# Performance work log

Measured on AMD Instinct MI355X. Metric: run time of the kernel, lower is better.

The kernel has to match this reference:

```python
import jax, jax.numpy as jnp
import numpy as np

B, T, A, FA = 4, 1024, 8, 16   # batch, frames, animals, per-animal feat
C, H, L = 1024, 16, 8          # n_embd, n_head, n_layer
D_IN, D_OUT = A * FA, 256


def _ln(x, g, b, eps=1e-5):
    mu = x.mean(-1, keepdims=True)
    var = ((x - mu) ** 2).mean(-1, keepdims=True)
    return (x - mu) * jax.lax.rsqrt(var + eps) * g + b


def setup_inputs() -> dict:
    key = jax.random.key(0)
    ks = iter(jax.random.split(key, 32))
    w = lambda shape: jax.random.normal(next(ks), shape, jnp.float32) * 0.02
    inp = {
        'tokens': jax.random.normal(next(ks), (B, T, A, FA), jnp.float32),
        'tok_emb_w': w((D_IN, C)), 'tok_emb_b': jnp.zeros((C,), jnp.float32),
        # per-layer params stacked along leading n_layer axis
        'ln1_g': jnp.ones((L, C), jnp.float32), 'ln1_b': jnp.zeros((L, C), jnp.float32),
        'Wq': w((L, C, C)), 'bq': jnp.zeros((L, C), jnp.float32),
        'Wk': w((L, C, C)), 'bk': jnp.zeros((L, C), jnp.float32),
        'Wv': w((L, C, C)), 'bv': jnp.zeros((L, C), jnp.float32),
        'Wo': w((L, C, C)), 'bo': jnp.zeros((L, C), jnp.float32),
        'ln2_g': jnp.ones((L, C), jnp.float32), 'ln2_b': jnp.zeros((L, C), jnp.float32),
        'W1': w((L, C, 4 * C)), 'b1': jnp.zeros((L, 4 * C), jnp.float32),
        'W2': w((L, 4 * C, C)), 'b2': jnp.zeros((L, C), jnp.float32),
        'lnf_g': jnp.ones((C,), jnp.float32), 'lnf_b': jnp.zeros((C,), jnp.float32),
        'proj_w': w((C, D_OUT)), 'proj_b': jnp.zeros((D_OUT,), jnp.float32),
        'dec_w1': w((D_OUT, D_OUT)), 'dec_b1': jnp.zeros((D_OUT,), jnp.float32),
        'dec_ln_g': jnp.ones((D_OUT,), jnp.float32), 'dec_ln_b': jnp.zeros((D_OUT,), jnp.float32),
        'dec_w2': w((D_OUT, D_IN)), 'dec_b2': jnp.zeros((D_IN,), jnp.float32),
    }
    return inp


def reference(tokens, tok_emb_w, tok_emb_b, ln1_g, ln1_b, Wq, bq, Wk, bk, Wv, bv,
              Wo, bo, ln2_g, ln2_b, W1, b1, W2, b2, lnf_g, lnf_b, proj_w, proj_b,
              dec_w1, dec_b1, dec_ln_g, dec_ln_b, dec_w2, dec_b2):
    b, t = tokens.shape[0], tokens.shape[1]
    x = tokens.reshape(b, t, -1)                      # (B,T,D_IN) flatten(2)
    h = x @ tok_emb_w + tok_emb_b                     # (B,T,C)
    mask = jnp.tril(jnp.ones((t, t), bool))           # causal mask
    dh = C // H
    scale = 1.0 / np.sqrt(dh)

    def layer(h, p):
        g1, bb1, wq, bq_, wk, bk_, wv, bv_, wo, bo_, g2, bb2, w1, b1_, w2, b2_ = p
        a = _ln(h, g1, bb1)
        q = (a @ wq + bq_).reshape(b, t, H, dh).transpose(0, 2, 1, 3)
        k = (a @ wk + bk_).reshape(b, t, H, dh).transpose(0, 2, 1, 3)
        v = (a @ wv + bv_).reshape(b, t, H, dh).transpose(0, 2, 1, 3)
        att = jnp.einsum('bhqd,bhkd->bhqk', q, k) * scale
        att = jnp.where(mask, att, -jnp.inf)
        att = jax.nn.softmax(att, axis=-1)
        y = jnp.einsum('bhqk,bhkd->bhqd', att, v)
        y = y.transpose(0, 2, 1, 3).reshape(b, t, C)
        h = h + (y @ wo + bo_)
        m = _ln(h, g2, bb2)
        h = h + jax.nn.gelu(m @ w1 + b1_, approximate=False) @ w2 + b2_
        return h, None

    h, _ = jax.lax.scan(layer, h, (ln1_g, ln1_b, Wq, bq, Wk, bk, Wv, bv, Wo, bo,
                                   ln2_g, ln2_b, W1, b1, W2, b2))
    feats = _ln(h, lnf_g, lnf_b) @ proj_w + proj_b    # (B,T,D_OUT)
    # decode=True path: decoder_frame then frame-delta prediction
    pred = _ln(jnp.tanh(feats @ dec_w1 + dec_b1), dec_ln_g, dec_ln_b) @ dec_w2 + dec_b2
    return pred[:, :-1] - x[:, 1:]                    # (B,T-1,D_IN)
```

## Files before the change

### kernel.cpp

```cpp
#include <hip/hip_runtime.h>
#include <hip/hip_bf16.h>

typedef unsigned short u16;
typedef __attribute__((ext_vector_type(8))) short bf16x8;
typedef __attribute__((ext_vector_type(4))) float f32x4;

#define BT     4096
#define CDIM   1024
#define NH     16
#define FF     4096
#define DIN    128
#define DOUT   256
#define NLAYER 8
#define TSEQ   1024
#define NBATCH 4

__device__ inline u16 f2bfu(float v) {
    __hip_bfloat16 h = __float2bfloat16(v);
    return __builtin_bit_cast(unsigned short, h);
}

__device__ inline void async_copy16(const u16* g, u16* l) {
    __builtin_amdgcn_global_load_lds((const __attribute__((address_space(1))) void*)g,
                                     (__attribute__((address_space(3))) void*)l,
                                     16, 0, 0);
}

template<int ACT, int RES, int OBF>
__global__ __launch_bounds__(256) void gemm_bt(
    const u16* __restrict__ A, const u16* __restrict__ Bt,
    const float* __restrict__ bias, const float* res,
    void* outp, int M, int N, int K)
{
    __shared__ __align__(16) u16 As[128 * 32];
    __shared__ __align__(16) u16 Bs[128 * 32];
    int tid  = threadIdx.x;
    int wave = tid >> 6, lane = tid & 63;
    int ln = lane & 15, quad = lane >> 4;
    int wm = (wave >> 1) * 64, wn = (wave & 1) * 64;
    const u16* Ab = A  + (size_t)blockIdx.y * 128 * K;
    const u16* Bb = Bt + (size_t)blockIdx.x * 128 * K;
    f32x4 acc[4][4] = {};
    for (int kt = 0; kt < K; kt += 32) {
#pragma unroll
        for (int it = 0; it < 2; ++it) {
            int e = it * 256 + tid;
            int row = e >> 2, col = (e & 3) * 8;
            int lbase = (it * 256 + wave * 64) * 8;
            async_copy16(Ab + (size_t)row * K + kt + col, As + lbase);
            async_copy16(Bb + (size_t)row * K + kt + col, Bs + lbase);
        }
        __syncthreads();
        bf16x8 af[4], bfr[4];
#pragma unroll
        for (int i = 0; i < 4; ++i)
            af[i] = *(const bf16x8*)&As[(wm + i * 16 + ln) * 32 + quad * 8];
#pragma unroll
        for (int j = 0; j < 4; ++j)
            bfr[j] = *(const bf16x8*)&Bs[(wn + j * 16 + ln) * 32 + quad * 8];
#pragma unroll
        for (int i = 0; i < 4; ++i)
#pragma unroll
            for (int j = 0; j < 4; ++j)
                acc[i][j] = __builtin_amdgcn_mfma_f32_16x16x32_bf16(af[i], bfr[j], acc[i][j], 0, 0, 0);
        __syncthreads();
    }
    int gr0 = blockIdx.y * 128 + wm + quad * 4;
    int gc0 = blockIdx.x * 128 + wn + ln;
#pragma unroll
    for (int i = 0; i < 4; ++i) {
#pragma unroll
        for (int j = 0; j < 4; ++j) {
            int gc = gc0 + j * 16;
            float bv = bias[gc];
#pragma unroll
            for (int r = 0; r < 4; ++r) {
                int gr = gr0 + i * 16 + r;
                float v = acc[i][j][r] + bv;
                if (ACT == 1) v = 0.5f * v * (1.0f + erff(v * 0.70710678118654752f));
                if (ACT == 2) v = tanhf(v);
                size_t idx = (size_t)gr * N + gc;
                if (RES) v += res[idx];
                if (OBF) ((u16*)outp)[idx] = f2bfu(v);
                else     ((float*)outp)[idx] = v;
            }
        }
    }
}

__global__ __launch_bounds__(64) void attn_kernel(const u16* __restrict__ qkv, u16* __restrict__ y)
{
    __shared__ __align__(16) u16 Plds[16 * 32];
    int qt = blockIdx.x, bh = blockIdx.y;
    int b = bh >> 4, h = bh & 15;
    int q0 = qt * 16;
    int lane = threadIdx.x;
    int ln = lane & 15, quad = lane >> 4;
    const int SC = 3 * CDIM;
    const u16* base = qkv + (size_t)b * TSEQ * SC;
    const u16* qrow = base + (size_t)(q0 + ln) * SC + h * 64 + quad * 8;
    bf16x8 qf0 = *(const bf16x8*)(qrow);
    bf16x8 qf1 = *(const bf16x8*)(qrow + 32);
    f32x4 O[4] = {};
    float m_i[4], l_i[4];
#pragma unroll
    for (int r = 0; r < 4; ++r) { m_i[r] = -1e30f; l_i[r] = 0.0f; }
    int nkt = qt / 2 + 1;
    for (int kt = 0; kt < nkt; ++kt) {
        int j0 = kt * 32;
        const u16* krow0 = base + (size_t)(j0 + ln) * SC + CDIM + h * 64;
        const u16* krow1 = base + (size_t)(j0 + 16 + ln) * SC + CDIM + h * 64;
        bf16x8 kf00 = *(const bf16x8*)(krow0 + quad * 8);
        bf16x8 kf01 = *(const bf16x8*)(krow0 + 32 + quad * 8);
        bf16x8 kf10 = *(const bf16x8*)(krow1 + quad * 8);
        bf16x8 kf11 = *(const bf16x8*)(krow1 + 32 + quad * 8);
        f32x4 S0 = {}, S1 = {};
        S0 = __builtin_amdgcn_mfma_f32_16x16x32_bf16(qf0, kf00, S0, 0, 0, 0);
        S0 = __builtin_amdgcn_mfma_f32_16x16x32_bf16(qf1, kf01, S0, 0, 0, 0);
        S1 = __builtin_amdgcn_mfma_f32_16x16x32_bf16(qf0, kf10, S1, 0, 0, 0);
        S1 = __builtin_amdgcn_mfma_f32_16x16x32_bf16(qf1, kf11, S1, 0, 0, 0);
        bool needmask = (j0 + 32 > q0);
        float alpha[4];
#pragma unroll
        for (int r = 0; r < 4; ++r) {
            float s0 = S0[r] * 0.125f, s1 = S1[r] * 0.125f;
            if (needmask) {
                int qr = q0 + quad * 4 + r;
                if (j0 + ln > qr)      s0 = -1e30f;
                if (j0 + 16 + ln > qr) s1 = -1e30f;
            }
            float mx = fmaxf(s0, s1);
            mx = fmaxf(mx, __shfl_xor(mx, 1));
            mx = fmaxf(mx, __shfl_xor(mx, 2));
            mx = fmaxf(mx, __shfl_xor(mx, 4));
            mx = fmaxf(mx, __shfl_xor(mx, 8));
            float mn = fmaxf(m_i[r], mx);
            float al = __expf(m_i[r] - mn);
            float p0 = __expf(s0 - mn);
            float p1 = __expf(s1 - mn);
            float rs = p0 + p1;
            rs += __shfl_xor(rs, 1);
            rs += __shfl_xor(rs, 2);
            rs += __shfl_xor(rs, 4);
            rs += __shfl_xor(rs, 8);
            l_i[r] = l_i[r] * al + rs;
            m_i[r] = mn;
            alpha[r] = al;
            Plds[(quad * 4 + r) * 32 + ln]      = f2bfu(p0);
            Plds[(quad * 4 + r) * 32 + 16 + ln] = f2bfu(p1);
        }
#pragma unroll
        for (int nt = 0; nt < 4; ++nt)
#pragma unroll
            for (int r = 0; r < 4; ++r)
                O[nt][r] *= alpha[r];
        __syncthreads();
        bf16x8 pa = *(const bf16x8*)&Plds[ln * 32 + quad * 8];
        const u16* vrow = base + (size_t)(j0 + quad * 8) * SC + 2 * CDIM + h * 64 + ln;
#pragma unroll
        for (int nt = 0; nt < 4; ++nt) {
            bf16x8 vf;
#pragma unroll
            for (int jj = 0; jj < 8; ++jj)
                vf[jj] = (short)vrow[(size_t)jj * SC + nt * 16];
            O[nt] = __builtin_amdgcn_mfma_f32_16x16x32_bf16(pa, vf, O[nt], 0, 0, 0);
        }
        __syncthreads();
    }
#pragma unroll
    for (int r = 0; r < 4; ++r) {
        float invl = 1.0f / l_i[r];
        int row = q0 + quad * 4 + r;
#pragma unroll
        for (int nt = 0; nt < 4; ++nt)
            y[(size_t)(b * TSEQ + row) * CDIM + h * 64 + nt * 16 + ln] = f2bfu(O[nt][r] * invl);
    }
}

template<int NPT>
__global__ __launch_bounds__(256) void ln_kernel(const float* __restrict__ x,
    const float* __restrict__ g, const float* __restrict__ bet, u16* __restrict__ out)
{
    const int n = NPT * 256;
    int row = blockIdx.x, tid = threadIdx.x;
    const float* xr = x + (size_t)row * n;
    float xv[NPT];
    float s1 = 0.f, s2 = 0.f;
#pragma unroll
    for (int k = 0; k < NPT; ++k) {
        float v = xr[k * 256 + tid];
        xv[k] = v; s1 += v; s2 += v * v;
    }
#pragma unroll
    for (int m = 1; m < 64; m <<= 1) { s1 += __shfl_xor(s1, m); s2 += __shfl_xor(s2, m); }
    __shared__ float red[8];
    int wv = tid >> 6;
    if ((tid & 63) == 0) { red[wv] = s1; red[4 + wv] = s2; }
    __syncthreads();
    s1 = red[0] + red[1] + red[2] + red[3];
    s2 = red[4] + red[5] + red[6] + red[7];
    float mu = s1 * (1.0f / n);
    float var = s2 * (1.0f / n) - mu * mu;
    float rs = rsqrtf(var + 1e-5f);
#pragma unroll
    for (int k = 0; k < NPT; ++k) {
        int c = k * 256 + tid;
        out[(size_t)row * n + c] = f2bfu((xv[k] - mu) * rs * g[c] + bet[c]);
    }
}

__device__ inline void tile_tc(const float* src, u16* dst, int K, int N, int kt, int nt,
                               int tid, float* sm)
{
    int c = tid & 31, r0 = tid >> 5;
#pragma unroll
    for (int rr = r0; rr < 32; rr += 8)
        sm[rr * 33 + c] = src[(size_t)(kt * 32 + rr) * N + nt * 32 + c];
    __syncthreads();
#pragma unroll
    for (int rr = r0; rr < 32; rr += 8)
        dst[(size_t)(nt * 32 + rr) * K + kt * 32 + c] = f2bfu(sm[c * 33 + rr]);
}

__global__ __launch_bounds__(256) void transpose_cvt(const float* __restrict__ src,
    u16* __restrict__ dst, int K, int N)
{
    __shared__ float sm[32 * 33];
    tile_tc(src, dst, K, N, blockIdx.y, blockIdx.x, threadIdx.x, sm);
}

__global__ __launch_bounds__(256) void prep_layer(
    const float* __restrict__ Wq, const float* __restrict__ Wk, const float* __restrict__ Wv,
    const float* __restrict__ Wo, const float* __restrict__ W1, const float* __restrict__ W2,
    const float* __restrict__ bq, const float* __restrict__ bk, const float* __restrict__ bv,
    u16* __restrict__ qkv_t, u16* __restrict__ wo_t, u16* __restrict__ w1_t,
    u16* __restrict__ w2_t, float* __restrict__ bias3)
{
    __shared__ float sm[32 * 33];
    int id = blockIdx.x, tid = threadIdx.x;
    const float* src; u16* dst; int K, N, kt, nt;
    if (id < 3072) {
        int w = id >> 10, t = id & 1023;
        src = (w == 0) ? Wq : ((w == 1) ? Wk : Wv);
        dst = qkv_t + (size_t)w * CDIM * CDIM;
        K = CDIM; N = CDIM; kt = t >> 5; nt = t & 31;
    } else if (id < 4096) {
        int t = id - 3072; src = Wo; dst = wo_t; K = CDIM; N = CDIM; kt = t >> 5; nt = t & 31;
    } else if (id < 8192) {
        int t = id - 4096; src = W1; dst = w1_t; K = CDIM; N = FF;   kt = t >> 7; nt = t & 127;
    } else {
        int t = id - 8192; src = W2; dst = w2_t; K = FF;   N = CDIM; kt = t >> 5; nt = t & 31;
    }
    tile_tc(src, dst, K, N, kt, nt, tid, sm);
    if (id < 3) {
        const float* bsrc = (id == 0) ? bq : ((id == 1) ? bk : bv);
        for (int k2 = tid; k2 < CDIM; k2 += 256) bias3[id * CDIM + k2] = bsrc[k2];
    }
}

__global__ __launch_bounds__(256) void cvt_bf16(const float* __restrict__ src,
    u16* __restrict__ dst, int n)
{
    int i = blockIdx.x * 256 + threadIdx.x;
    if (i < n) dst[i] = f2bfu(src[i]);
}

__global__ __launch_bounds__(256) void out_sub(const float* __restrict__ pred,
    const float* __restrict__ x, float* __restrict__ out, int total)
{
    int i = blockIdx.x * 256 + threadIdx.x;
    if (i >= total) return;
    int b = i / ((TSEQ - 1) * DIN);
    int rtmp = i - b * (TSEQ - 1) * DIN;
    int t = rtmp >> 7, f = rtmp & 127;
    out[i] = pred[(size_t)(b * TSEQ + t) * DIN + f] - x[(size_t)(b * TSEQ + t + 1) * DIN + f];
}

__global__ void fail_flag(float* out) { if (threadIdx.x == 0 && blockIdx.x == 0) out[0] = 1.0e6f; }

extern "C" void kernel_launch(void* const* d_in, const int* in_sizes, int n_in,
                              void* d_out, int out_size, void* d_ws, size_t ws_size,
                              hipStream_t stream)
{
    (void)in_sizes; (void)n_in; (void)out_size;
    const float* tokens    = (const float*)d_in[0];
    const float* tok_emb_w = (const float*)d_in[1];
    const float* tok_emb_b = (const float*)d_in[2];
    const float* ln1_g = (const float*)d_in[3];
    const float* ln1_b = (const float*)d_in[4];
    const float* Wq = (const float*)d_in[5];
    const float* bq = (const float*)d_in[6];
    const float* Wk = (const float*)d_in[7];
    const float* bk = (const float*)d_in[8];
    const float* Wv = (const float*)d_in[9];
    const float* bv = (const float*)d_in[10];
    const float* Wo = (const float*)d_in[11];
    const float* bo = (const float*)d_in[12];
    const float* ln2_g = (const float*)d_in[13];
    const float* ln2_b = (const float*)d_in[14];
    const float* W1 = (const float*)d_in[15];
    const float* b1 = (const float*)d_in[16];
    const float* W2 = (const float*)d_in[17];
    const float* b2 = (const float*)d_in[18];
    const float* lnf_g = (const float*)d_in[19];
    const float* lnf_b = (const float*)d_in[20];
    const float* proj_w = (const float*)d_in[21];
    const float* proj_b = (const float*)d_in[22];
    const float* dec_w1 = (const float*)d_in[23];
    const float* dec_b1 = (const float*)d_in[24];
    const float* dec_ln_g = (const float*)d_in[25];
    const float* dec_ln_b = (const float*)d_in[26];
    const float* dec_w2 = (const float*)d_in[27];
    const float* dec_b2 = (const float*)d_in[28];

    char* p = (char*)d_ws;
    auto alloc = [&](size_t bytes) -> char* {
        char* r = p; p += (bytes + 255) & ~(size_t)255; return r;
    };
    u16*   xb     = (u16*)  alloc((size_t)BT * DIN * 2);
    float* h      = (float*)alloc((size_t)BT * CDIM * 4);
    u16*   abuf   = (u16*)  alloc((size_t)BT * CDIM * 2);
    u16*   qkvb   = (u16*)  alloc((size_t)BT * 3 * CDIM * 2);
    u16*   yb     = (u16*)  alloc((size_t)BT * CDIM * 2);
    u16*   t1     = (u16*)  alloc((size_t)BT * FF * 2);
    u16*   feats  = (u16*)  alloc((size_t)BT * DOUT * 2);
    float* d1     = (float*)alloc((size_t)BT * DOUT * 4);
    u16*   d1n    = (u16*)  alloc((size_t)BT * DOUT * 2);
    float* pred   = (float*)alloc((size_t)BT * DIN * 4);
    u16*   emb_t  = (u16*)  alloc((size_t)CDIM * DIN * 2);
    u16*   proj_t = (u16*)  alloc((size_t)DOUT * CDIM * 2);
    u16*   dec1_t = (u16*)  alloc((size_t)DOUT * DOUT * 2);
    u16*   dec2_t = (u16*)  alloc((size_t)DIN * DOUT * 2);
    u16*   qkv_t  = (u16*)  alloc((size_t)3 * CDIM * CDIM * 2);
    u16*   wo_t   = (u16*)  alloc((size_t)CDIM * CDIM * 2);
    u16*   w1_t   = (u16*)  alloc((size_t)FF * CDIM * 2);
    u16*   w2_t   = (u16*)  alloc((size_t)CDIM * FF * 2);
    float* bias3  = (float*)alloc((size_t)3 * CDIM * 4);
    if ((size_t)(p - (char*)d_ws) > ws_size) {
        fail_flag<<<1, 64, 0, stream>>>((float*)d_out);
        return;
    }

    cvt_bf16<<<(BT * DIN) / 256, 256, 0, stream>>>(tokens, xb, BT * DIN);
    transpose_cvt<<<dim3(CDIM / 32, DIN / 32),  256, 0, stream>>>(tok_emb_w, emb_t,  DIN,  CDIM);
    transpose_cvt<<<dim3(DOUT / 32, CDIM / 32), 256, 0, stream>>>(proj_w,    proj_t, CDIM, DOUT);
    transpose_cvt<<<dim3(DOUT / 32, DOUT / 32), 256, 0, stream>>>(dec_w1,    dec1_t, DOUT, DOUT);
    transpose_cvt<<<dim3(DIN / 32,  DOUT / 32), 256, 0, stream>>>(dec_w2,    dec2_t, DOUT, DIN);
    gemm_bt<0, 0, 0><<<dim3(CDIM / 128, BT / 128), 256, 0, stream>>>(
        xb, emb_t, tok_emb_b, nullptr, h, BT, CDIM, DIN);

    for (int l = 0; l < NLAYER; ++l) {
        prep_layer<<<12288, 256, 0, stream>>>(
            Wq + (size_t)l * CDIM * CDIM, Wk + (size_t)l * CDIM * CDIM,
            Wv + (size_t)l * CDIM * CDIM, Wo + (size_t)l * CDIM * CDIM,
            W1 + (size_t)l * CDIM * FF,   W2 + (size_t)l * FF * CDIM,
            bq + l * CDIM, bk + l * CDIM, bv + l * CDIM,
            qkv_t, wo_t, w1_t, w2_t, bias3);
        ln_kernel<4><<<BT, 256, 0, stream>>>(h, ln1_g + l * CDIM, ln1_b + l * CDIM, abuf);
        gemm_bt<0, 0, 1><<<dim3(3 * CDIM / 128, BT / 128), 256, 0, stream>>>(
            abuf, qkv_t, bias3, nullptr, qkvb, BT, 3 * CDIM, CDIM);
        attn_kernel<<<dim3(TSEQ / 16, NBATCH * NH), 64, 0, stream>>>(qkvb, yb);
        gemm_bt<0, 1, 0><<<dim3(CDIM / 128, BT / 128), 256, 0, stream>>>(
            yb, wo_t, bo + l * CDIM, h, h, BT, CDIM, CDIM);
        ln_kernel<4><<<BT, 256, 0, stream>>>(h, ln2_g + l * CDIM, ln2_b + l * CDIM, abuf);
        gemm_bt<1, 0, 1><<<dim3(FF / 128, BT / 128), 256, 0, stream>>>(
            abuf, w1_t, b1 + l * FF, nullptr, t1, BT, FF, CDIM);
        gemm_bt<0, 1, 0><<<dim3(CDIM / 128, BT / 128), 256, 0, stream>>>(
            t1, w2_t, b2 + l * CDIM, h, h, BT, CDIM, FF);
    }

    ln_kernel<4><<<BT, 256, 0, stream>>>(h, lnf_g, lnf_b, abuf);
    gemm_bt<0, 0, 1><<<dim3(DOUT / 128, BT / 128), 256, 0, stream>>>(
        abuf, proj_t, proj_b, nullptr, feats, BT, DOUT, CDIM);
    gemm_bt<2, 0, 0><<<dim3(DOUT / 128, BT / 128), 256, 0, stream>>>(
        feats, dec1_t, dec_b1, nullptr, d1, BT, DOUT, DOUT);
    ln_kernel<1><<<BT, 256, 0, stream>>>(d1, dec_ln_g, dec_ln_b, d1n);
    gemm_bt<0, 0, 0><<<dim3(DIN / 128, BT / 128), 256, 0, stream>>>(
        d1n, dec2_t, dec_b2, nullptr, pred, BT, DIN, DOUT);
    int total = NBATCH * (TSEQ - 1) * DIN;
    out_sub<<<(total + 255) / 256, 256, 0, stream>>>(pred, tokens, (float*)d_out, total);
}
```

Baseline: 3.264 ms.

## Split-K atomics for residual GEMMs, transposed V layout, 32-row attention tiles

```diff
diff --git a/kernel.cpp b/kernel.cpp
--- a/kernel.cpp
+++ b/kernel.cpp
@@ -26,11 +26,11 @@
                                      16, 0, 0);
 }
 
-template<int ACT, int RES, int OBF>
+template<int ACT, int RES, int OBF, int EPI>
 __global__ __launch_bounds__(256) void gemm_bt(
     const u16* __restrict__ A, const u16* __restrict__ Bt,
     const float* __restrict__ bias, const float* res,
-    void* outp, int M, int N, int K)
+    void* outp, u16* __restrict__ vtp, int N, int K, int Kc)
 {
     __shared__ __align__(16) u16 As[128 * 32];
     __shared__ __align__(16) u16 Bs[128 * 32];
@@ -38,10 +38,11 @@
     int wave = tid >> 6, lane = tid & 63;
     int ln = lane & 15, quad = lane >> 4;
     int wm = (wave >> 1) * 64, wn = (wave & 1) * 64;
+    int k0 = blockIdx.z * Kc;
     const u16* Ab = A  + (size_t)blockIdx.y * 128 * K;
     const u16* Bb = Bt + (size_t)blockIdx.x * 128 * K;
     f32x4 acc[4][4] = {};
-    for (int kt = 0; kt < K; kt += 32) {
+    for (int kt = k0; kt < k0 + Kc; kt += 32) {
 #pragma unroll
         for (int it = 0; it < 2; ++it) {
             int e = it * 256 + tid;
@@ -72,109 +73,136 @@
 #pragma unroll
         for (int j = 0; j < 4; ++j) {
             int gc = gc0 + j * 16;
-            float bv = bias[gc];
+            float bv = (EPI == 1) ? ((blockIdx.z == 0) ? bias[gc] : 0.0f) : bias[gc];
 #pragma unroll
             for (int r = 0; r < 4; ++r) {
                 int gr = gr0 + i * 16 + r;
                 float v = acc[i][j][r] + bv;
                 if (ACT == 1) v = 0.5f * v * (1.0f + erff(v * 0.70710678118654752f));
                 if (ACT == 2) v = tanhf(v);
-                size_t idx = (size_t)gr * N + gc;
-                if (RES) v += res[idx];
-                if (OBF) ((u16*)outp)[idx] = f2bfu(v);
-                else     ((float*)outp)[idx] = v;
+                if (EPI == 1) {
+                    unsafeAtomicAdd(&((float*)outp)[(size_t)gr * N + gc], v);
+                } else if (EPI == 2) {
+                    if ((int)blockIdx.x < 16) {
+                        ((u16*)outp)[(size_t)gr * 2048 + gc] = f2bfu(v);
+                    } else {
+                        int c2 = gc - 2048;
+                        int hh = c2 >> 6, f = c2 & 63;
+                        int bb = gr >> 10, t = gr & 1023;
+                        vtp[((size_t)(bb * 16 + hh) * 64 + f) * TSEQ + t] = f2bfu(v);
+                    }
+                } else {
+                    size_t idx = (size_t)gr * N + gc;
+                    if (RES) v += res[idx];
+                    if (OBF) ((u16*)outp)[idx] = f2bfu(v);
+                    else     ((float*)outp)[idx] = v;
+                }
             }
         }
     }
 }
 
-__global__ __launch_bounds__(64) void attn_kernel(const u16* __restrict__ qkv, u16* __restrict__ y)
-{
-    __shared__ __align__(16) u16 Plds[16 * 32];
+__global__ __launch_bounds__(64) void attn_kernel(const u16* __restrict__ qk,
+    const u16* __restrict__ vT, u16* __restrict__ y)
+{
+    __shared__ __align__(16) u16 Plds[2][16 * 32];
     int qt = blockIdx.x, bh = blockIdx.y;
     int b = bh >> 4, h = bh & 15;
-    int q0 = qt * 16;
+    int q0 = qt * 32;
     int lane = threadIdx.x;
     int ln = lane & 15, quad = lane >> 4;
-    const int SC = 3 * CDIM;
-    const u16* base = qkv + (size_t)b * TSEQ * SC;
-    const u16* qrow = base + (size_t)(q0 + ln) * SC + h * 64 + quad * 8;
-    bf16x8 qf0 = *(const bf16x8*)(qrow);
-    bf16x8 qf1 = *(const bf16x8*)(qrow + 32);
-    f32x4 O[4] = {};
-    float m_i[4], l_i[4];
-#pragma unroll
-    for (int r = 0; r < 4; ++r) { m_i[r] = -1e30f; l_i[r] = 0.0f; }
-    int nkt = qt / 2 + 1;
+    const u16* qbase = qk + (size_t)b * TSEQ * 2048;
+    bf16x8 qf[2][2];
+#pragma unroll
+    for (int qi = 0; qi < 2; ++qi) {
+        const u16* qrow = qbase + (size_t)(q0 + qi * 16 + ln) * 2048 + h * 64 + quad * 8;
+        qf[qi][0] = *(const bf16x8*)qrow;
+        qf[qi][1] = *(const bf16x8*)(qrow + 32);
+    }
+    const u16* vbase = vT + (size_t)bh * 64 * TSEQ;
+    f32x4 O[2][4] = {};
+    float m_i[2][4], l_i[2][4];
+#pragma unroll
+    for (int qi = 0; qi < 2; ++qi)
+#pragma unroll
+        for (int r = 0; r < 4; ++r) { m_i[qi][r] = -1e30f; l_i[qi][r] = 0.0f; }
+    int nkt = qt + 1;
     for (int kt = 0; kt < nkt; ++kt) {
         int j0 = kt * 32;
-        const u16* krow0 = base + (size_t)(j0 + ln) * SC + CDIM + h * 64;
-        const u16* krow1 = base + (size_t)(j0 + 16 + ln) * SC + CDIM + h * 64;
-        bf16x8 kf00 = *(const bf16x8*)(krow0 + quad * 8);
-        bf16x8 kf01 = *(const bf16x8*)(krow0 + 32 + quad * 8);
-        bf16x8 kf10 = *(const bf16x8*)(krow1 + quad * 8);
-        bf16x8 kf11 = *(const bf16x8*)(krow1 + 32 + quad * 8);
-        f32x4 S0 = {}, S1 = {};
-        S0 = __builtin_amdgcn_mfma_f32_16x16x32_bf16(qf0, kf00, S0, 0, 0, 0);
-        S0 = __builtin_amdgcn_mfma_f32_16x16x32_bf16(qf1, kf01, S0, 0, 0, 0);
-        S1 = __builtin_amdgcn_mfma_f32_16x16x32_bf16(qf0, kf10, S1, 0, 0, 0);
-        S1 = __builtin_amdgcn_mfma_f32_16x16x32_bf16(qf1, kf11, S1, 0, 0, 0);
-        bool needmask = (j0 + 32 > q0);
-        float alpha[4];
+        bf16x8 kf[2][2];
+#pragma unroll
+        for (int kk = 0; kk < 2; ++kk) {
+            const u16* krow = qbase + (size_t)(j0 + kk * 16 + ln) * 2048 + 1024 + h * 64 + quad * 8;
+            kf[kk][0] = *(const bf16x8*)krow;
+            kf[kk][1] = *(const bf16x8*)(krow + 32);
+        }
+        f32x4 S[2][2] = {};
+#pragma unroll
+        for (int qi = 0; qi < 2; ++qi)
+#pragma unroll
+            for (int kk = 0; kk < 2; ++kk) {
+                S[qi][kk] = __builtin_amdgcn_mfma_f32_16x16x32_bf16(qf[qi][0], kf[kk][0], S[qi][kk], 0, 0, 0);
+                S[qi][kk] = __builtin_amdgcn_mfma_f32_16x16x32_bf16(qf[qi][1], kf[kk][1], S[qi][kk], 0, 0, 0);
+            }
+        bool lastt = (kt == qt);
+        float alpha[2][4];
+#pragma unroll
+        for (int qi = 0; qi < 2; ++qi) {
+#pragma unroll
+            for (int r = 0; r < 4; ++r) {
+                float s0 = S[qi][0][r] * 0.125f, s1 = S[qi][1][r] * 0.125f;
+                if (lastt) {
+                    int qr = q0 + qi * 16 + quad * 4 + r;
+                    if (j0 + ln > qr)      s0 = -1e30f;
+                    if (j0 + 16 + ln > qr) s1 = -1e30f;
+                }
+                float mx = fmaxf(s0, s1);
+                mx = fmaxf(mx, __shfl_xor(mx, 1));
+                mx = fmaxf(mx, __shfl_xor(mx, 2));
+                mx = fmaxf(mx, __shfl_xor(mx, 4));
+                mx = fmaxf(mx, __shfl_xor(mx, 8));
+                float mn = fmaxf(m_i[qi][r], mx);
+                float al = __expf(m_i[qi][r] - mn);
+                float p0 = __expf(s0 - mn);
+                float p1 = __expf(s1 - mn);
+                float rs = p0 + p1;
+                rs += __shfl_xor(rs, 1);
+                rs += __shfl_xor(rs, 2);
+                rs += __shfl_xor(rs, 4);
+                rs += __shfl_xor(rs, 8);
+                l_i[qi][r] = l_i[qi][r] * al + rs;
+                m_i[qi][r] = mn;
+                alpha[qi][r] = al;
+                Plds[qi][(quad * 4 + r) * 32 + ln]      = f2bfu(p0);
+                Plds[qi][(quad * 4 + r) * 32 + 16 + ln] = f2bfu(p1);
+            }
+#pragma unroll
+            for (int nt = 0; nt < 4; ++nt)
+#pragma unroll
+                for (int r = 0; r < 4; ++r)
+                    O[qi][nt][r] *= alpha[qi][r];
+        }
+        __syncthreads();
+        bf16x8 pa0 = *(const bf16x8*)&Plds[0][ln * 32 + quad * 8];
+        bf16x8 pa1 = *(const bf16x8*)&Plds[1][ln * 32 + quad * 8];
+#pragma unroll
+        for (int nt = 0; nt < 4; ++nt) {
+            bf16x8 vf = *(const bf16x8*)(vbase + (size_t)(nt * 16 + ln) * TSEQ + j0 + quad * 8);
+            O[0][nt] = __builtin_amdgcn_mfma_f32_16x16x32_bf16(pa0, vf, O[0][nt], 0, 0, 0);
+            O[1][nt] = __builtin_amdgcn_mfma_f32_16x16x32_bf16(pa1, vf, O[1][nt], 0, 0, 0);
+        }
+        __syncthreads();
+    }
+#pragma unroll
+    for (int qi = 0; qi < 2; ++qi)
 #pragma unroll
         for (int r = 0; r < 4; ++r) {
-            float s0 = S0[r] * 0.125f, s1 = S1[r] * 0.125f;
-            if (needmask) {
-                int qr = q0 + quad * 4 + r;
-                if (j0 + ln > qr)      s0 = -1e30f;
-                if (j0 + 16 + ln > qr) s1 = -1e30f;
-            }
-            float mx = fmaxf(s0, s1);
-            mx = fmaxf(mx, __shfl_xor(mx, 1));
-            mx = fmaxf(mx, __shfl_xor(mx, 2));
-            mx = fmaxf(mx, __shfl_xor(mx, 4));
-            mx = fmaxf(mx, __shfl_xor(mx, 8));
-            float mn = fmaxf(m_i[r], mx);
-            float al = __expf(m_i[r] - mn);
-            float p0 = __expf(s0 - mn);
-            float p1 = __expf(s1 - mn);
-            float rs = p0 + p1;
-            rs += __shfl_xor(rs, 1);
-            rs += __shfl_xor(rs, 2);
-            rs += __shfl_xor(rs, 4);
-            rs += __shfl_xor(rs, 8);
-            l_i[r] = l_i[r] * al + rs;
-            m_i[r] = mn;
-            alpha[r] = al;
-            Plds[(quad * 4 + r) * 32 + ln]      = f2bfu(p0);
-            Plds[(quad * 4 + r) * 32 + 16 + ln] = f2bfu(p1);
-        }
-#pragma unroll
-        for (int nt = 0; nt < 4; ++nt)
-#pragma unroll
-            for (int r = 0; r < 4; ++r)
-                O[nt][r] *= alpha[r];
-        __syncthreads();
-        bf16x8 pa = *(const bf16x8*)&Plds[ln * 32 + quad * 8];
-        const u16* vrow = base + (size_t)(j0 + quad * 8) * SC + 2 * CDIM + h * 64 + ln;
-#pragma unroll
-        for (int nt = 0; nt < 4; ++nt) {
-            bf16x8 vf;
-#pragma unroll
-            for (int jj = 0; jj < 8; ++jj)
-                vf[jj] = (short)vrow[(size_t)jj * SC + nt * 16];
-            O[nt] = __builtin_amdgcn_mfma_f32_16x16x32_bf16(pa, vf, O[nt], 0, 0, 0);
-        }
-        __syncthreads();
-    }
-#pragma unroll
-    for (int r = 0; r < 4; ++r) {
-        float invl = 1.0f / l_i[r];
-        int row = q0 + quad * 4 + r;
-#pragma unroll
-        for (int nt = 0; nt < 4; ++nt)
-            y[(size_t)(b * TSEQ + row) * CDIM + h * 64 + nt * 16 + ln] = f2bfu(O[nt][r] * invl);
-    }
+            float invl = 1.0f / l_i[qi][r];
+            int row = q0 + qi * 16 + quad * 4 + r;
+#pragma unroll
+            for (int nt = 0; nt < 4; ++nt)
+                y[(size_t)(b * TSEQ + row) * CDIM + h * 64 + nt * 16 + ln] = f2bfu(O[qi][nt][r] * invl);
+        }
 }
 
 template<int NPT>
@@ -263,6 +291,12 @@
 {
     int i = blockIdx.x * 256 + threadIdx.x;
     if (i < n) dst[i] = f2bfu(src[i]);
+}
+
+__global__ __launch_bounds__(256) void zero_f32(float* __restrict__ dst, int n)
+{
+    int i = blockIdx.x * 256 + threadIdx.x;
+    if (i < n) dst[i] = 0.0f;
 }
 
 __global__ __launch_bounds__(256) void out_sub(const float* __restrict__ pred,
@@ -317,25 +351,27 @@
     auto alloc = [&](size_t bytes) -> char* {
         char* r = p; p += (bytes + 255) & ~(size_t)255; return r;
     };
-    u16*   xb     = (u16*)  alloc((size_t)BT * DIN * 2);
-    float* h      = (float*)alloc((size_t)BT * CDIM * 4);
-    u16*   abuf   = (u16*)  alloc((size_t)BT * CDIM * 2);
-    u16*   qkvb   = (u16*)  alloc((size_t)BT * 3 * CDIM * 2);
-    u16*   yb     = (u16*)  alloc((size_t)BT * CDIM * 2);
-    u16*   t1     = (u16*)  alloc((size_t)BT * FF * 2);
-    u16*   feats  = (u16*)  alloc((size_t)BT * DOUT * 2);
-    float* d1     = (float*)alloc((size_t)BT * DOUT * 4);
-    u16*   d1n    = (u16*)  alloc((size_t)BT * DOUT * 2);
-    float* pred   = (float*)alloc((size_t)BT * DIN * 4);
-    u16*   emb_t  = (u16*)  alloc((size_t)CDIM * DIN * 2);
-    u16*   proj_t = (u16*)  alloc((size_t)DOUT * CDIM * 2);
-    u16*   dec1_t = (u16*)  alloc((size_t)DOUT * DOUT * 2);
-    u16*   dec2_t = (u16*)  alloc((size_t)DIN * DOUT * 2);
-    u16*   qkv_t  = (u16*)  alloc((size_t)3 * CDIM * CDIM * 2);
-    u16*   wo_t   = (u16*)  alloc((size_t)CDIM * CDIM * 2);
-    u16*   w1_t   = (u16*)  alloc((size_t)FF * CDIM * 2);
-    u16*   w2_t   = (u16*)  alloc((size_t)CDIM * FF * 2);
-    float* bias3  = (float*)alloc((size_t)3 * CDIM * 4);
+    u16*   xb      = (u16*)  alloc((size_t)BT * DIN * 2);
+    float* h       = (float*)alloc((size_t)BT * CDIM * 4);
+    u16*   abuf    = (u16*)  alloc((size_t)BT * CDIM * 2);
+    u16*   qkb     = (u16*)  alloc((size_t)BT * 2048 * 2);
+    u16*   vTb     = (u16*)  alloc((size_t)NBATCH * NH * 64 * TSEQ * 2);
+    u16*   yb      = (u16*)  alloc((size_t)BT * CDIM * 2);
+    u16*   t1      = (u16*)  alloc((size_t)BT * FF * 2);
+    u16*   feats   = (u16*)  alloc((size_t)BT * DOUT * 2);
+    float* projacc = (float*)alloc((size_t)BT * DOUT * 4);
+    float* d1      = (float*)alloc((size_t)BT * DOUT * 4);
+    u16*   d1n     = (u16*)  alloc((size_t)BT * DOUT * 2);
+    float* pred    = (float*)alloc((size_t)BT * DIN * 4);
+    u16*   emb_t   = (u16*)  alloc((size_t)CDIM * DIN * 2);
+    u16*   proj_t  = (u16*)  alloc((size_t)DOUT * CDIM * 2);
+    u16*   dec1_t  = (u16*)  alloc((size_t)DOUT * DOUT * 2);
+    u16*   dec2_t  = (u16*)  alloc((size_t)DIN * DOUT * 2);
+    u16*   qkv_t   = (u16*)  alloc((size_t)3 * CDIM * CDIM * 2);
+    u16*   wo_t    = (u16*)  alloc((size_t)CDIM * CDIM * 2);
+    u16*   w1_t    = (u16*)  alloc((size_t)FF * CDIM * 2);
+    u16*   w2_t    = (u16*)  alloc((size_t)CDIM * FF * 2);
+    float* bias3   = (float*)alloc((size_t)3 * CDIM * 4);
     if ((size_t)(p - (char*)d_ws) > ws_size) {
         fail_flag<<<1, 64, 0, stream>>>((float*)d_out);
         return;
@@ -346,8 +382,8 @@
     transpose_cvt<<<dim3(DOUT / 32, CDIM / 32), 256, 0, stream>>>(proj_w,    proj_t, CDIM, DOUT);
     transpose_cvt<<<dim3(DOUT / 32, DOUT / 32), 256, 0, stream>>>(dec_w1,    dec1_t, DOUT, DOUT);
     transpose_cvt<<<dim3(DIN / 32,  DOUT / 32), 256, 0, stream>>>(dec_w2,    dec2_t, DOUT, DIN);
-    gemm_bt<0, 0, 0><<<dim3(CDIM / 128, BT / 128), 256, 0, stream>>>(
-        xb, emb_t, tok_emb_b, nullptr, h, BT, CDIM, DIN);
+    gemm_bt<0, 0, 0, 0><<<dim3(CDIM / 128, BT / 128, 1), 256, 0, stream>>>(
+        xb, emb_t, tok_emb_b, nullptr, h, nullptr, CDIM, DIN, DIN);
 
     for (int l = 0; l < NLAYER; ++l) {
         prep_layer<<<12288, 256, 0, stream>>>(
@@ -357,26 +393,28 @@
             bq + l * CDIM, bk + l * CDIM, bv + l * CDIM,
             qkv_t, wo_t, w1_t, w2_t, bias3);
         ln_kernel<4><<<BT, 256, 0, stream>>>(h, ln1_g + l * CDIM, ln1_b + l * CDIM, abuf);
-        gemm_bt<0, 0, 1><<<dim3(3 * CDIM / 128, BT / 128), 256, 0, stream>>>(
-            abuf, qkv_t, bias3, nullptr, qkvb, BT, 3 * CDIM, CDIM);
-        attn_kernel<<<dim3(TSEQ / 16, NBATCH * NH), 64, 0, stream>>>(qkvb, yb);
-        gemm_bt<0, 1, 0><<<dim3(CDIM / 128, BT / 128), 256, 0, stream>>>(
-            yb, wo_t, bo + l * CDIM, h, h, BT, CDIM, CDIM);
+        gemm_bt<0, 0, 1, 2><<<dim3(3 * CDIM / 128, BT / 128, 1), 256, 0, stream>>>(
+            abuf, qkv_t, bias3, nullptr, qkb, vTb, 3 * CDIM, CDIM, CDIM);
+        attn_kernel<<<dim3(TSEQ / 32, NBATCH * NH), 64, 0, stream>>>(qkb, vTb, yb);
+        gemm_bt<0, 0, 0, 1><<<dim3(CDIM / 128, BT / 128, 2), 256, 0, stream>>>(
+            yb, wo_t, bo + l * CDIM, nullptr, h, nullptr, CDIM, CDIM, CDIM / 2);
         ln_kernel<4><<<BT, 256, 0, stream>>>(h, ln2_g + l * CDIM, ln2_b + l * CDIM, abuf);
-        gemm_bt<1, 0, 1><<<dim3(FF / 128, BT / 128), 256, 0, stream>>>(
-            abuf, w1_t, b1 + l * FF, nullptr, t1, BT, FF, CDIM);
-        gemm_bt<0, 1, 0><<<dim3(CDIM / 128, BT / 128), 256, 0, stream>>>(
-            t1, w2_t, b2 + l * CDIM, h, h, BT, CDIM, FF);
+        gemm_bt<1, 0, 1, 0><<<dim3(FF / 128, BT / 128, 1), 256, 0, stream>>>(
+            abuf, w1_t, b1 + l * FF, nullptr, t1, nullptr, FF, CDIM, CDIM);
+        gemm_bt<0, 0, 0, 1><<<dim3(CDIM / 128, BT / 128, 2), 256, 0, stream>>>(
+            t1, w2_t, b2 + l * CDIM, nullptr, h, nullptr, CDIM, FF, FF / 2);
     }
 
     ln_kernel<4><<<BT, 256, 0, stream>>>(h, lnf_g, lnf_b, abuf);
-    gemm_bt<0, 0, 1><<<dim3(DOUT / 128, BT / 128), 256, 0, stream>>>(
-        abuf, proj_t, proj_b, nullptr, feats, BT, DOUT, CDIM);
-    gemm_bt<2, 0, 0><<<dim3(DOUT / 128, BT / 128), 256, 0, stream>>>(
-        feats, dec1_t, dec_b1, nullptr, d1, BT, DOUT, DOUT);
+    zero_f32<<<(BT * DOUT) / 256, 256, 0, stream>>>(projacc, BT * DOUT);
+    gemm_bt<0, 0, 0, 1><<<dim3(DOUT / 128, BT / 128, 4), 256, 0, stream>>>(
+        abuf, proj_t, proj_b, nullptr, projacc, nullptr, DOUT, CDIM, CDIM / 4);
+    cvt_bf16<<<(BT * DOUT) / 256, 256, 0, stream>>>(projacc, feats, BT * DOUT);
+    gemm_bt<2, 0, 0, 0><<<dim3(DOUT / 128, BT / 128, 1), 256, 0, stream>>>(
+        feats, dec1_t, dec_b1, nullptr, d1, nullptr, DOUT, DOUT, DOUT);
     ln_kernel<1><<<BT, 256, 0, stream>>>(d1, dec_ln_g, dec_ln_b, d1n);
-    gemm_bt<0, 0, 0><<<dim3(DIN / 128, BT / 128), 256, 0, stream>>>(
-        d1n, dec2_t, dec_b2, nullptr, pred, BT, DIN, DOUT);
+    gemm_bt<0, 0, 0, 0><<<dim3(DIN / 128, BT / 128, 1), 256, 0, stream>>>(
+        d1n, dec2_t, dec_b2, nullptr, pred, nullptr, DIN, DOUT, DOUT);
     int total = NBATCH * (TSEQ - 1) * DIN;
     out_sub<<<(total + 255) / 256, 256, 0, stream>>>(pred, tokens, (float*)d_out, total);
 }
```

After: 3.137 ms. -3.9%, faster.
